# Optimization experiments

Measured on AMD Instinct MI355X. Metric: run time of the kernel, lower is better.

Reference implementation:

```python
import jax, jax.numpy as jnp
import numpy as np

N_GAUSS, H, W, SH_DEG = 1024, 256, 256, 3

SH_C0 = 0.28209479177387814
SH_C1 = 0.4886025119029199
SH_C2 = (1.0925484305920792, -1.0925484305920792, 0.31539156525252005,
         -1.0925484305920792, 0.5462742152960396)
SH_C3 = (-0.5900435899266435, 2.890611442640554, -0.4570457994644658,
         0.3731763325901154, -0.4570457994644658, 1.445305721320277,
         -0.5900435899266435)


def eval_sh(shs, dirs):
    # shs: [N,16,3], dirs: [N,3] normalized. Matches computeColorFromSH (deg 3).
    x, y, z = dirs[:, 0:1], dirs[:, 1:2], dirs[:, 2:3]
    res = SH_C0 * shs[:, 0]
    res = res - SH_C1 * y * shs[:, 1] + SH_C1 * z * shs[:, 2] - SH_C1 * x * shs[:, 3]
    xx, yy, zz = x * x, y * y, z * z
    xy, yz, xz = x * y, y * z, x * z
    res = (res + SH_C2[0] * xy * shs[:, 4] + SH_C2[1] * yz * shs[:, 5]
           + SH_C2[2] * (2.0 * zz - xx - yy) * shs[:, 6]
           + SH_C2[3] * xz * shs[:, 7] + SH_C2[4] * (xx - yy) * shs[:, 8])
    res = (res + SH_C3[0] * y * (3.0 * xx - yy) * shs[:, 9]
           + SH_C3[1] * xy * z * shs[:, 10]
           + SH_C3[2] * y * (4.0 * zz - xx - yy) * shs[:, 11]
           + SH_C3[3] * z * (2.0 * zz - 3.0 * xx - 3.0 * yy) * shs[:, 12]
           + SH_C3[4] * x * (4.0 * zz - xx - yy) * shs[:, 13]
           + SH_C3[5] * z * (xx - yy) * shs[:, 14]
           + SH_C3[6] * x * (xx - yy - zz) * shs[:, 15])
    return jnp.maximum(res + 0.5, 0.0)


def render(background, means3D, opacities, scales, rotations, shs,
           view_mat, proj_mat, cam_pos, tan_fovx, tan_fovy, height, width):
    N = means3D.shape[0]
    tanx, tany = tan_fovx[0], tan_fovy[0]
    fx = width / (2.0 * tanx)
    fy = height / (2.0 * tany)

    # --- 3D covariance: Sigma = R diag(s^2) R^T (computeCov3D) ---
    q = rotations / jnp.linalg.norm(rotations, axis=-1, keepdims=True)
    r, x, y, z = q[:, 0], q[:, 1], q[:, 2], q[:, 3]
    R = jnp.stack([
        jnp.stack([1 - 2 * (y * y + z * z), 2 * (x * y - r * z), 2 * (x * z + r * y)], -1),
        jnp.stack([2 * (x * y + r * z), 1 - 2 * (x * x + z * z), 2 * (y * z - r * x)], -1),
        jnp.stack([2 * (x * z - r * y), 2 * (y * z + r * x), 1 - 2 * (x * x + y * y)], -1),
    ], -2)  # [N,3,3]
    M = R * scales[:, None, :]
    Sigma = jnp.einsum('nij,nkj->nik', M, M)  # [N,3,3]

    # --- view transform + EWA 2D covariance (computeCov2D) ---
    t = means3D @ view_mat[:3, :3].T + view_mat[:3, 3]  # [N,3] camera space
    tz = t[:, 2]
    valid_z = tz > 0.2
    tzs = jnp.where(valid_z, tz, 1.0)
    limx, limy = 1.3 * tanx, 1.3 * tany
    tx = jnp.clip(t[:, 0] / tzs, -limx, limx) * tzs
    ty = jnp.clip(t[:, 1] / tzs, -limy, limy) * tzs
    zeros = jnp.zeros_like(tzs)
    J = jnp.stack([
        jnp.stack([fx / tzs, zeros, -fx * tx / (tzs * tzs)], -1),
        jnp.stack([zeros, fy / tzs, -fy * ty / (tzs * tzs)], -1),
    ], -2)  # [N,2,3]
    T2 = jnp.einsum('nij,jk->nik', J, view_mat[:3, :3])
    cov2d = jnp.einsum('nij,njk,nlk->nil', T2, Sigma, T2)  # [N,2,2]
    a = cov2d[:, 0, 0] + 0.3
    c = cov2d[:, 1, 1] + 0.3
    b = cov2d[:, 0, 1]
    det = a * c - b * b
    valid = valid_z & (det > 0)
    inv_det = jnp.where(det > 0, 1.0 / jnp.where(det > 0, det, 1.0), 0.0)
    conic = jnp.stack([c, -b, a], -1) * inv_det[:, None]  # [N,3]

    # --- projection to pixel coords (ndc2Pix) ---
    ph = jnp.concatenate([means3D, jnp.ones((N, 1), means3D.dtype)], -1) @ proj_mat.T
    p_w = 1.0 / (ph[:, 3] + 1e-7)
    px = ((ph[:, 0] * p_w + 1.0) * width - 1.0) * 0.5
    py = ((ph[:, 1] * p_w + 1.0) * height - 1.0) * 0.5

    # --- SH -> RGB ---
    dirs = means3D - cam_pos[None, :]
    dirs = dirs / jnp.linalg.norm(dirs, axis=-1, keepdims=True)
    colors = eval_sh(shs, dirs)  # [N,3]

    # --- global depth sort (front to back) ---
    depth = jnp.where(valid, tz, 1e10)
    order = jnp.argsort(depth)
    px_s, py_s = px[order], py[order]
    conic_s = conic[order]
    opac_s = opacities[order, 0]
    colors_s = colors[order]
    valid_s = valid[order]

    # --- per-pixel alpha and front-to-back compositing (renderCUDA) ---
    ys, xs = jnp.meshgrid(jnp.arange(height, dtype=jnp.float32),
                          jnp.arange(width, dtype=jnp.float32), indexing='ij')
    pixx, pixy = xs.reshape(-1), ys.reshape(-1)  # [P]
    dx = px_s[:, None] - pixx[None, :]  # [N,P]
    dy = py_s[:, None] - pixy[None, :]
    power = (-0.5 * (conic_s[:, 0:1] * dx * dx + conic_s[:, 2:3] * dy * dy)
             - conic_s[:, 1:2] * dx * dy)
    alpha = jnp.minimum(opac_s[:, None] * jnp.exp(jnp.minimum(power, 0.0)), 0.99)
    keep = (power <= 0.0) & (alpha >= 1.0 / 255.0) & valid_s[:, None]
    alpha = jnp.where(keep, alpha, 0.0)

    Tcum = jnp.cumprod(1.0 - alpha, axis=0)  # [N,P]
    T_prev = jnp.concatenate([jnp.ones((1, alpha.shape[1]), alpha.dtype), Tcum[:-1]], 0)
    wgt = alpha * T_prev
    img = jnp.einsum('nc,np->cp', colors_s, wgt) + background[:, None] * Tcum[-1][None, :]
    return img.reshape(3, height, width)


def setup_inputs() -> dict:
    key = jax.random.key(0)
    ks = jax.random.split(key, 6)
    means3D = jax.random.uniform(ks[0], (N_GAUSS, 3), minval=-3.0, maxval=3.0)
    means3D = means3D.at[:, 2].set(
        jax.random.uniform(ks[1], (N_GAUSS,), minval=2.0, maxval=10.0))
    opacities = jax.random.uniform(ks[2], (N_GAUSS, 1), minval=0.3, maxval=0.95)
    scales = jax.random.uniform(ks[3], (N_GAUSS, 3), minval=0.02, maxval=0.15)
    rotations = jax.random.normal(ks[4], (N_GAUSS, 4))
    shs = jax.random.normal(ks[5], (N_GAUSS, (SH_DEG + 1) ** 2, 3)) * 0.3
    background = jnp.zeros((3,), jnp.float32)
    view_mat = jnp.eye(4, dtype=jnp.float32)  # camera at origin looking +z
    tanx = tany = 0.5
    zn, zf = 0.01, 100.0
    proj = np.zeros((4, 4), np.float32)
    proj[0, 0] = 1.0 / tanx
    proj[1, 1] = 1.0 / tany
    proj[2, 2] = zf / (zf - zn)
    proj[2, 3] = -(zf * zn) / (zf - zn)
    proj[3, 2] = 1.0
    proj_mat = jnp.asarray(proj) @ view_mat  # full projection
    cam_pos = jnp.zeros((3,), jnp.float32)
    return dict(background=background, means3D=means3D, opacities=opacities,
                scales=scales, rotations=rotations, shs=shs, view_mat=view_mat,
                proj_mat=proj_mat, cam_pos=cam_pos,
                tan_fovx=jnp.array([tanx], jnp.float32),
                tan_fovy=jnp.array([tany], jnp.float32), height=H, width=W)


def reference(background, means3D, opacities, scales, rotations, shs,
              view_mat, proj_mat, cam_pos, tan_fovx, tan_fovy, height, width):
    return render(background, means3D, opacities, scales, rotations, shs,
                  view_mat, proj_mat, cam_pos, tan_fovx, tan_fovy, height, width)
```

## Files before the change

### kernel.cpp

```cpp
#include <hip/hip_runtime.h>
#include <math.h>

#define NG 1024
#define LOG2E 1.4426950408889634f


__global__ void prep_kernel(
    const float* __restrict__ means3D, const float* __restrict__ opacities,
    const float* __restrict__ scales,  const float* __restrict__ rotations,
    const float* __restrict__ shs,     const float* __restrict__ view_mat,
    const float* __restrict__ proj_mat,const float* __restrict__ cam_pos,
    const float* __restrict__ tanx_p,  const float* __restrict__ tany_p,
    const int* __restrict__ h_p,       const int* __restrict__ w_p,
    float* __restrict__ depth, float4* __restrict__ bbox,
    float4* __restrict__ rec, int N)
{
    int i = blockIdx.x * blockDim.x + threadIdx.x;
    if (i >= N) return;
    float tanx = tanx_p[0], tany = tany_p[0];
    float Wf = (float)w_p[0], Hf = (float)h_p[0];
    float fx = Wf / (2.f * tanx), fy = Hf / (2.f * tany);

    float mx = means3D[3*i], my = means3D[3*i+1], mz = means3D[3*i+2];

    float qr = rotations[4*i],   qx = rotations[4*i+1];
    float qy = rotations[4*i+2], qz = rotations[4*i+3];
    float qn = sqrtf(qr*qr + qx*qx + qy*qy + qz*qz);
    qr /= qn; qx /= qn; qy /= qn; qz /= qn;
    float sx = scales[3*i], sy = scales[3*i+1], sz = scales[3*i+2];
    float R00 = 1.f-2.f*(qy*qy+qz*qz), R01 = 2.f*(qx*qy-qr*qz), R02 = 2.f*(qx*qz+qr*qy);
    float R10 = 2.f*(qx*qy+qr*qz), R11 = 1.f-2.f*(qx*qx+qz*qz), R12 = 2.f*(qy*qz-qr*qx);
    float R20 = 2.f*(qx*qz-qr*qy), R21 = 2.f*(qy*qz+qr*qx), R22 = 1.f-2.f*(qx*qx+qy*qy);
    float M00=R00*sx, M01=R01*sy, M02=R02*sz;
    float M10=R10*sx, M11=R11*sy, M12=R12*sz;
    float M20=R20*sx, M21=R21*sy, M22=R22*sz;
    float S00 = M00*M00+M01*M01+M02*M02;
    float S01 = M00*M10+M01*M11+M02*M12;
    float S02 = M00*M20+M01*M21+M02*M22;
    float S11 = M10*M10+M11*M11+M12*M12;
    float S12 = M10*M20+M11*M21+M12*M22;
    float S22 = M20*M20+M21*M21+M22*M22;

    const float* V = view_mat;
    float t0 = V[0]*mx + V[1]*my + V[2]*mz  + V[3];
    float t1 = V[4]*mx + V[5]*my + V[6]*mz  + V[7];
    float t2 = V[8]*mx + V[9]*my + V[10]*mz + V[11];
    bool valid_z = t2 > 0.2f;
    float tzs = valid_z ? t2 : 1.0f;
    float limx = 1.3f*tanx, limy = 1.3f*tany;
    float txc = fminf(fmaxf(t0/tzs, -limx), limx) * tzs;
    float tyc = fminf(fmaxf(t1/tzs, -limy), limy) * tzs;
    float inv_tz = 1.f / tzs;
    float J00 = fx*inv_tz, J02 = -fx*txc*inv_tz*inv_tz;
    float J11 = fy*inv_tz, J12 = -fy*tyc*inv_tz*inv_tz;
    float T200 = J00*V[0] + J02*V[8];
    float T201 = J00*V[1] + J02*V[9];
    float T202 = J00*V[2] + J02*V[10];
    float T210 = J11*V[4] + J12*V[8];
    float T211 = J11*V[5] + J12*V[9];
    float T212 = J11*V[6] + J12*V[10];
    float u0 = S00*T200 + S01*T201 + S02*T202;
    float u1 = S01*T200 + S11*T201 + S12*T202;
    float u2 = S02*T200 + S12*T201 + S22*T202;
    float cov00 = T200*u0 + T201*u1 + T202*u2;
    float cov01 = T210*u0 + T211*u1 + T212*u2;
    float v0 = S00*T210 + S01*T211 + S02*T212;
    float v1 = S01*T210 + S11*T211 + S12*T212;
    float v2 = S02*T210 + S12*T211 + S22*T212;
    float cov11 = T210*v0 + T211*v1 + T212*v2;
    float a = cov00 + 0.3f;
    float c = cov11 + 0.3f;
    float b = cov01;
    float det = a*c - b*b;
    bool valid = valid_z && (det > 0.f);
    float inv_det = (det > 0.f) ? (1.f/det) : 0.f;
    float Aq = c*inv_det, Bq = -b*inv_det, Cq = a*inv_det;

    const float* P = proj_mat;
    float ph0 = P[0]*mx  + P[1]*my  + P[2]*mz  + P[3];
    float ph1 = P[4]*mx  + P[5]*my  + P[6]*mz  + P[7];
    float ph3 = P[12]*mx + P[13]*my + P[14]*mz + P[15];
    float pw = 1.f / (ph3 + 1e-7f);
    float px = ((ph0*pw + 1.f)*Wf - 1.f)*0.5f;
    float py = ((ph1*pw + 1.f)*Hf - 1.f)*0.5f;

    float dxm = mx - cam_pos[0], dym = my - cam_pos[1], dzm = mz - cam_pos[2];
    float dn = sqrtf(dxm*dxm + dym*dym + dzm*dzm);
    float X = dxm/dn, Y = dym/dn, Z = dzm/dn;
    float xx = X*X, yy = Y*Y, zz = Z*Z;
    float xy = X*Y, yz = Y*Z, xz = X*Z;
    float col[3];
    #pragma unroll
    for (int ch = 0; ch < 3; ch++) {
        const float* s = shs + i*48 + ch;
        float res = 0.28209479177387814f * s[0];
        res += -0.4886025119029199f * Y * s[3]
             +  0.4886025119029199f * Z * s[6]
             -  0.4886025119029199f * X * s[9];
        res +=  1.0925484305920792f * xy * s[12]
             + (-1.0925484305920792f) * yz * s[15]
             +  0.31539156525252005f * (2.f*zz - xx - yy) * s[18]
             + (-1.0925484305920792f) * xz * s[21]
             +  0.5462742152960396f * (xx - yy) * s[24];
        res += -0.5900435899266435f * Y * (3.f*xx - yy) * s[27]
             +  2.890611442640554f  * xy * Z * s[30]
             + (-0.4570457994644658f) * Y * (4.f*zz - xx - yy) * s[33]
             +  0.3731763325901154f  * Z * (2.f*zz - 3.f*xx - 3.f*yy) * s[36]
             + (-0.4570457994644658f) * X * (4.f*zz - xx - yy) * s[39]
             +  1.445305721320277f   * Z * (xx - yy) * s[42]
             + (-0.5900435899266435f) * X * (xx - yy - zz) * s[45];
        col[ch] = fmaxf(res + 0.5f, 0.f);
    }

    float op = valid ? opacities[i] : 0.f;
    depth[i] = valid ? t2 : 1e10f;

    float tau = 2.f * logf(255.f * fmaxf(op, 1e-20f));
    bool has = valid && (op * 255.f > 1.f) && (tau > 0.f);
    float rx = has ? (sqrtf(tau * a) + 0.01f) : 0.f;
    float ry = has ? (sqrtf(tau * c) + 0.01f) : 0.f;
    bbox[i] = has ? make_float4(px - rx, py - ry, px + rx, py + ry)
                  : make_float4(1e9f, 1e9f, -1e9f, -1e9f);

    rec[i*3 + 0] = make_float4(px, py, -0.5f*LOG2E*Aq, -LOG2E*Bq);
    rec[i*3 + 1] = make_float4(-0.5f*LOG2E*Cq, op, col[0], col[1]);
    rec[i*3 + 2] = make_float4(col[2], 0.f, 0.f, 0.f);
}

__device__ inline unsigned long long bstage_shfl(unsigned long long key,
                                                 int tid, int j, int k) {
    unsigned long long partner = __shfl_xor(key, j, 64);
    bool lower = (tid & j) == 0;
    bool asc   = (tid & k) == 0;
    return ((key < partner) == (lower == asc)) ? key : partner;
}

__global__ void __launch_bounds__(64) render_kernel(
    const float* __restrict__ depth,
    const float4* __restrict__ bbox,
    const float4* __restrict__ rec,
    const float* __restrict__ background,
    float* __restrict__ out,
    int N, int W, int HW)
{
    __shared__ unsigned long long skey[NG];
    int tile = blockIdx.x;
    int tilesX = W >> 3;
    int tx = tile % tilesX, ty = tile / tilesX;
    int lane = threadIdx.x;
    int lx = lane & 7, ly = lane >> 3;
    float pixx = (float)(tx*8 + lx);
    float pixy = (float)(ty*8 + ly);
    float x0 = (float)(tx*8), x1 = x0 + 7.f;
    float y0 = (float)(ty*8), y1 = y0 + 7.f;

    int cnt = 0;
    for (int base = 0; base < N; base += 64) {
        int gi = base + lane;
        bool hit = false;
        float dz = 0.f;
        if (gi < N) {
            float4 bb = bbox[gi];
            dz = depth[gi];
            hit = (bb.x <= x1) & (bb.z >= x0) & (bb.y <= y1) & (bb.w >= y0);
        }
        unsigned long long mask = __ballot(hit);
        if (hit) {
            int pos = cnt + __popcll(mask & ((1ull << lane) - 1ull));
            skey[pos] = ((unsigned long long)__float_as_uint(dz) << 32) | (unsigned)gi;
        }
        cnt += __popcll(mask);
    }
    __syncthreads();

    float T = 1.f, Cr = 0.f, Cg = 0.f, Cb = 0.f;
    if (cnt > 0) {
        if (cnt <= 64) {
            unsigned long long key = (lane < cnt) ? skey[lane] : ~0ull;
            for (int k = 2; k <= 64; k <<= 1)
                for (int j = k >> 1; j >= 1; j >>= 1)
                    key = bstage_shfl(key, lane, j, k);
            skey[lane] = key;
            __syncthreads();
        } else {
            int P = 128;
            while (P < cnt) P <<= 1;
            for (int i2 = cnt + lane; i2 < P; i2 += 64) skey[i2] = ~0ull;
            __syncthreads();
            for (int k = 2; k <= P; k <<= 1) {
                for (int j = k >> 1; j >= 1; j >>= 1) {
                    for (int i2 = lane; i2 < P; i2 += 64) {
                        int ixj = i2 ^ j;
                        if (ixj > i2) {
                            bool asc = (i2 & k) == 0;
                            unsigned long long u = skey[i2], v = skey[ixj];
                            if ((u > v) == asc) { skey[i2] = v; skey[ixj] = u; }
                        }
                    }
                    __syncthreads();
                }
            }
        }

        for (int h = 0; h < cnt; h++) {
            int gg = __builtin_amdgcn_readfirstlane((int)(unsigned)skey[h]);
            float4 r0 = rec[gg*3 + 0];
            float4 r1 = rec[gg*3 + 1];
            float4 r2 = rec[gg*3 + 2];
            float dx = r0.x - pixx, dy = r0.y - pixy;
            float p2 = fmaf(r0.z, dx*dx, fmaf(r1.x, dy*dy, r0.w*(dx*dy)));
            float e  = __builtin_amdgcn_exp2f(p2);
            float alpha = fminf(r1.y * e, 0.99f);
            float a2 = (alpha >= (1.f/255.f)) ? alpha : 0.f;
            float w = a2 * T;
            Cr = fmaf(r1.z, w, Cr);
            Cg = fmaf(r1.w, w, Cg);
            Cb = fmaf(r2.x, w, Cb);
            T  = T - a2 * T;
            if (__all(T < 1e-4f)) break;
        }
    }

    int p = (ty*8 + ly) * W + tx*8 + lx;
    out[p]        = Cr + background[0]*T;
    out[HW + p]   = Cg + background[1]*T;
    out[2*HW + p] = Cb + background[2]*T;
}

extern "C" void kernel_launch(void* const* d_in, const int* in_sizes, int n_in,
                              void* d_out, int out_size, void* d_ws, size_t ws_size,
                              hipStream_t stream) {
    const float* background = (const float*)d_in[0];
    const float* means3D    = (const float*)d_in[1];
    const float* opacities  = (const float*)d_in[2];
    const float* scales     = (const float*)d_in[3];
    const float* rotations  = (const float*)d_in[4];
    const float* shs        = (const float*)d_in[5];
    const float* view_mat   = (const float*)d_in[6];
    const float* proj_mat   = (const float*)d_in[7];
    const float* cam_pos    = (const float*)d_in[8];
    const float* tanx       = (const float*)d_in[9];
    const float* tany       = (const float*)d_in[10];
    const int*   hp         = (const int*)d_in[11];
    const int*   wp         = (const int*)d_in[12];

    int N  = in_sizes[2];
    int HW = out_size / 3;
    int W  = 256;
    int H  = HW / W;
    float* out = (float*)d_out;

    float*  depth = (float*)d_ws;
    float4* bbox  = (float4*)(depth + NG);
    float4* rec   = bbox + NG;

    prep_kernel<<<16, 64, 0, stream>>>(
        means3D, opacities, scales, rotations, shs, view_mat, proj_mat,
        cam_pos, tanx, tany, hp, wp, depth, bbox, rec, N);

    int tiles = (W >> 3) * (H >> 3);
    render_kernel<<<tiles, 64, 0, stream>>>(
        depth, bbox, rec, background, out, N, W, HW);
}
```

Before: 22.71 us.

## Batch-load gaussian records per wave and broadcast via readlane in blend loop

The blend loop previously issued three dependent uniform global loads per gaussian. It now loads up to 64 sorted gaussians' records in parallel, one per lane, and broadcasts each field with readlane inside an inner loop. This takes global load latency off the serial compositing chain. The prep kernel now also precomputes the 64-bit depth|index sort keys so the culling pass copies them directly, and the early-exit vote runs every 16 gaussians instead of every one. In exchange, a few extra gaussians are evaluated after saturation and each step issues more readlane instructions.

Measured after the change: 20.56 us. 1.1x faster.

```diff
diff --git a/kernel.cpp b/kernel.cpp
--- a/kernel.cpp
+++ b/kernel.cpp
@@ -12,7 +12,7 @@
     const float* __restrict__ proj_mat,const float* __restrict__ cam_pos,
     const float* __restrict__ tanx_p,  const float* __restrict__ tany_p,
     const int* __restrict__ h_p,       const int* __restrict__ w_p,
-    float* __restrict__ depth, float4* __restrict__ bbox,
+    unsigned long long* __restrict__ keys, float4* __restrict__ bbox,
     float4* __restrict__ rec, int N)
 {
     int i = blockIdx.x * blockDim.x + threadIdx.x;
@@ -113,7 +113,8 @@
     }
 
     float op = valid ? opacities[i] : 0.f;
-    depth[i] = valid ? t2 : 1e10f;
+    float dpt = valid ? t2 : 1e10f;
+    keys[i] = ((unsigned long long)__float_as_uint(dpt) << 32) | (unsigned)i;
 
     float tau = 2.f * logf(255.f * fmaxf(op, 1e-20f));
     bool has = valid && (op * 255.f > 1.f) && (tau > 0.f);
@@ -135,8 +136,12 @@
     return ((key < partner) == (lower == asc)) ? key : partner;
 }
 
+__device__ inline float rlane(float v, int l) {
+    return __int_as_float(__builtin_amdgcn_readlane(__float_as_int(v), l));
+}
+
 __global__ void __launch_bounds__(64) render_kernel(
-    const float* __restrict__ depth,
+    const unsigned long long* __restrict__ keys,
     const float4* __restrict__ bbox,
     const float4* __restrict__ rec,
     const float* __restrict__ background,
@@ -158,16 +163,16 @@
     for (int base = 0; base < N; base += 64) {
         int gi = base + lane;
         bool hit = false;
-        float dz = 0.f;
+        unsigned long long k = 0;
         if (gi < N) {
             float4 bb = bbox[gi];
-            dz = depth[gi];
+            k = keys[gi];
             hit = (bb.x <= x1) & (bb.z >= x0) & (bb.y <= y1) & (bb.w >= y0);
         }
         unsigned long long mask = __ballot(hit);
         if (hit) {
             int pos = cnt + __popcll(mask & ((1ull << lane) - 1ull));
-            skey[pos] = ((unsigned long long)__float_as_uint(dz) << 32) | (unsigned)gi;
+            skey[pos] = k;
         }
         cnt += __popcll(mask);
     }
@@ -202,22 +207,33 @@
             }
         }
 
-        for (int h = 0; h < cnt; h++) {
-            int gg = __builtin_amdgcn_readfirstlane((int)(unsigned)skey[h]);
+        bool dead = false;
+        for (int c = 0; c < cnt && !dead; c += 64) {
+            int len = min(64, cnt - c);
+            int idx = c + lane;
+            int gg = (idx < cnt) ? (int)(unsigned)skey[idx] : 0;
             float4 r0 = rec[gg*3 + 0];
             float4 r1 = rec[gg*3 + 1];
             float4 r2 = rec[gg*3 + 2];
-            float dx = r0.x - pixx, dy = r0.y - pixy;
-            float p2 = fmaf(r0.z, dx*dx, fmaf(r1.x, dy*dy, r0.w*(dx*dy)));
-            float e  = __builtin_amdgcn_exp2f(p2);
-            float alpha = fminf(r1.y * e, 0.99f);
-            float a2 = (alpha >= (1.f/255.f)) ? alpha : 0.f;
-            float w = a2 * T;
-            Cr = fmaf(r1.z, w, Cr);
-            Cg = fmaf(r1.w, w, Cg);
-            Cb = fmaf(r2.x, w, Cb);
-            T  = T - a2 * T;
-            if (__all(T < 1e-4f)) break;
+            for (int m = 0; m < len; m++) {
+                float gpx = rlane(r0.x, m), gpy = rlane(r0.y, m);
+                float gA  = rlane(r0.z, m), gB  = rlane(r0.w, m);
+                float gC  = rlane(r1.x, m), gop = rlane(r1.y, m);
+                float gcr = rlane(r1.z, m), gcg = rlane(r1.w, m);
+                float gcb = rlane(r2.x, m);
+                float dx = gpx - pixx, dy = gpy - pixy;
+                float p2 = fmaf(gA, dx*dx, fmaf(gC, dy*dy, gB*(dx*dy)));
+                float e  = __builtin_amdgcn_exp2f(p2);
+                float alpha = fminf(gop * e, 0.99f);
+                float a2 = (alpha >= (1.f/255.f)) ? alpha : 0.f;
+                float w = a2 * T;
+                Cr = fmaf(gcr, w, Cr);
+                Cg = fmaf(gcg, w, Cg);
+                Cb = fmaf(gcb, w, Cb);
+                T  = T - a2 * T;
+                if ((m & 15) == 15 && __all(T < 1e-4f)) { dead = true; break; }
+            }
+            if (__all(T < 1e-4f)) dead = true;
         }
     }
 
@@ -250,15 +266,15 @@
     int H  = HW / W;
     float* out = (float*)d_out;
 
-    float*  depth = (float*)d_ws;
-    float4* bbox  = (float4*)(depth + NG);
-    float4* rec   = bbox + NG;
+    unsigned long long* keys = (unsigned long long*)d_ws;
+    float4* bbox = (float4*)(keys + NG);
+    float4* rec  = bbox + NG;
 
     prep_kernel<<<16, 64, 0, stream>>>(
         means3D, opacities, scales, rotations, shs, view_mat, proj_mat,
-        cam_pos, tanx, tany, hp, wp, depth, bbox, rec, N);
+        cam_pos, tanx, tany, hp, wp, keys, bbox, rec, N);
 
     int tiles = (W >> 3) * (H >> 3);
     render_kernel<<<tiles, 64, 0, stream>>>(
-        depth, bbox, rec, background, out, N, W, HW);
-}
+        keys, bbox, rec, background, out, N, W, HW);
+}
```
